# Kernel tuning notes

Measured on AMD Instinct MI355X. Metric: run time of the kernel, lower is better.

Reference implementation:

```python
import jax, jax.numpy as jnp
import numpy as np

NHEAD = 8

def setup_inputs() -> dict:
    key = jax.random.key(0)
    ks = jax.random.split(key, 6)
    b, n, d = 4, 1024, 512
    emb = jax.random.normal(ks[0], (b, n, d), dtype=jnp.float32)
    dirs = jax.random.normal(ks[1], (b, n, n, 3), dtype=jnp.float32)
    d_mask = jax.random.normal(ks[2], (b * NHEAD, n, n), dtype=jnp.float32) * 0.1
    W_proj = jax.random.normal(ks[3], (d, 3 * d), dtype=jnp.float32) / np.sqrt(d)
    b_proj = jnp.zeros((3 * d,), dtype=jnp.float32)
    w_force = jax.random.normal(ks[4], (d,), dtype=jnp.float32) / np.sqrt(d)
    b_force = jnp.zeros((1,), dtype=jnp.float32)
    return {"emb": emb, "dirs": dirs, "d_mask": d_mask, "W_proj": W_proj,
            "b_proj": b_proj, "w_force": w_force, "b_force": b_force}

def reference(emb, dirs, d_mask, W_proj, b_proj, w_force, b_force):
    b, n, d = emb.shape
    h = NHEAD
    dh = d // h
    scale = jnp.asarray(np.sqrt(d), emb.dtype)
    qkv = emb @ W_proj + b_proj                      # (b,n,3d)
    q, k, v = jnp.split(qkv, 3, axis=-1)
    q = q.reshape(b, n, h, dh).transpose(0, 2, 1, 3) / scale   # (b,h,n,dh)
    k = k.reshape(b, n, h, dh).transpose(0, 2, 1, 3)           # (b,h,n,dh)
    v = v.reshape(b, n, h, dh).transpose(0, 2, 1, 3)           # (b,h,n,dh)
    scores = jnp.einsum('bhid,bhjd->bhij', q, k) + d_mask.reshape(b, h, n, n)
    attn = jax.nn.softmax(scores, axis=-1)                     # (b,h,n,n); dropout in eval mode = identity
    # torch: (attn[...,None] * dirs[:,None]) @ v  materializes (b,h,n,n,3);
    # fused einsum computes the same per-axis weighted sum without it.
    xyz = jnp.einsum('bhij,bija,bhjd->biahd', attn, dirs, v)   # (b,n,3,h,dh)
    xyz = xyz.reshape(b, n, 3, d)
    out = jnp.einsum('bnad,d->bna', xyz, w_force) + b_force[0]  # (b,n,3)
    return out
```

## Files before the change

kernel.cpp:

```cpp
#include <hip/hip_runtime.h>
#include <hip/hip_bf16.h>

#define NH 8
#define BB 4
#define NN 1024
#define DD 512
#define DH 64
#define JSPLIT 8

typedef __bf16 bf16x8 __attribute__((ext_vector_type(8)));
typedef float f32x4 __attribute__((ext_vector_type(4)));

__device__ __forceinline__ unsigned short f2bf(float f) {
    union { float f; unsigned u; } v; v.f = f;
    unsigned u = v.u;
    unsigned r = u + 0x7FFFu + ((u >> 16) & 1u);
    return (unsigned short)(r >> 16);
}

__global__ __launch_bounds__(256) void k_prep(const float* __restrict__ W,
                                              const float* __restrict__ b_proj,
                                              const float* __restrict__ w_force,
                                              unsigned short* __restrict__ Wt,
                                              float* __restrict__ bias_eff,
                                              float* __restrict__ wv_eff,
                                              float* __restrict__ s_bias) {
    __shared__ float tile[32][33];
    int bx = blockIdx.x;
    int t = threadIdx.x;
    const float rscale = 0.044194173824159216f;
    if (bx < 512) {
        int c0 = (bx & 15) * 32;
        int n0 = (bx >> 4) * 32;
        for (int i = 0; i < 4; ++i) {
            int idx = t + i * 256;
            int r = idx >> 5, cn = idx & 31;
            tile[r][cn] = W[(c0 + r) * (3 * DD) + n0 + cn];
        }
        __syncthreads();
        for (int i = 0; i < 4; ++i) {
            int idx = t + i * 256;
            int nn = idx >> 5, cc = idx & 31;
            float v = tile[cc][nn];
            int n = n0 + nn;
            if (n < DD) v *= rscale;
            Wt[n * DD + c0 + cc] = f2bf(v);
        }
        if ((bx & 15) == 0 && t < 32) {
            int n = n0 + t;
            bias_eff[n] = b_proj[n] * (n < DD ? rscale : 1.0f);
        }
        return;
    }
    int wave = t >> 6, lane = t & 63;
    if (bx == 640) {
        if (wave == 0) {
            for (int hh = 0; hh < NH; ++hh) {
                float p = b_proj[2 * DD + hh * DH + lane] * w_force[hh * DH + lane];
                for (int off = 32; off; off >>= 1) p += __shfl_xor(p, off);
                if (lane == 0) s_bias[hh] = p;
            }
        }
        return;
    }
    int c = (bx - 512) * 4 + wave;
    const float* wr = W + (size_t)c * (3 * DD) + 2 * DD;
    #pragma unroll
    for (int hh = 0; hh < NH; ++hh) {
        float p = wr[hh * DH + lane] * w_force[hh * DH + lane];
        for (int off = 32; off; off >>= 1) p += __shfl_xor(p, off);
        if (lane == 0) wv_eff[c * 8 + hh] = p;
    }
}

__global__ __launch_bounds__(128) void k_s(const float* __restrict__ emb,
                                           const float* __restrict__ wv_eff,
                                           const float* __restrict__ s_bias,
                                           float* __restrict__ s_ws) {
    int t = blockIdx.x * 128 + threadIdx.x;
    int row = t >> 3;
    int h = t & 7;
    const float* er = emb + (size_t)row * DD;
    const float* wp = wv_eff + h;
    float acc = 0.f;
    #pragma unroll 8
    for (int c4 = 0; c4 < DD / 4; ++c4) {
        float4 e = *(const float4*)(er + c4 * 4);
        acc += e.x * wp[(c4 * 4 + 0) * 8];
        acc += e.y * wp[(c4 * 4 + 1) * 8];
        acc += e.z * wp[(c4 * 4 + 2) * 8];
        acc += e.w * wp[(c4 * 4 + 3) * 8];
    }
    int b = row >> 10, j = row & 1023;
    s_ws[(b * 8 + h) * NN + j] = acc + s_bias[h];
}

__global__ __launch_bounds__(256) void k_gemm(const float* __restrict__ emb,
                                              const unsigned short* __restrict__ Wt,
                                              const float* __restrict__ bias_eff,
                                              unsigned short* __restrict__ qb,
                                              unsigned short* __restrict__ kb) {
    __shared__ __align__(16) unsigned short a_s[128 * 32];
    __shared__ __align__(16) unsigned short b_s[128 * 32];
    int m0 = blockIdx.x * 128, n0 = blockIdx.y * 128;
    int t = threadIdx.x;
    int wave = t >> 6, lane = t & 63;
    int wr = (wave >> 1) * 64, wc = (wave & 1) * 64;
    int qd = lane >> 4, c = lane & 15;
    int sr = t >> 2, sg = (t & 3) * 8;
    f32x4 acc[4][4] = {};
    for (int k0 = 0; k0 < DD; k0 += 32) {
        float4 x0 = *(const float4*)(emb + (size_t)(m0 + sr) * DD + k0 + sg);
        float4 x1 = *(const float4*)(emb + (size_t)(m0 + sr) * DD + k0 + sg + 4);
        float4 y0 = *(const float4*)(emb + (size_t)(m0 + 64 + sr) * DD + k0 + sg);
        float4 y1 = *(const float4*)(emb + (size_t)(m0 + 64 + sr) * DD + k0 + sg + 4);
        uint4 bv0 = *(const uint4*)(Wt + (size_t)(n0 + sr) * DD + k0 + sg);
        uint4 bv1 = *(const uint4*)(Wt + (size_t)(n0 + 64 + sr) * DD + k0 + sg);
        union { unsigned short u[8]; uint4 v; } px, py;
        px.u[0] = f2bf(x0.x); px.u[1] = f2bf(x0.y); px.u[2] = f2bf(x0.z); px.u[3] = f2bf(x0.w);
        px.u[4] = f2bf(x1.x); px.u[5] = f2bf(x1.y); px.u[6] = f2bf(x1.z); px.u[7] = f2bf(x1.w);
        py.u[0] = f2bf(y0.x); py.u[1] = f2bf(y0.y); py.u[2] = f2bf(y0.z); py.u[3] = f2bf(y0.w);
        py.u[4] = f2bf(y1.x); py.u[5] = f2bf(y1.y); py.u[6] = f2bf(y1.z); py.u[7] = f2bf(y1.w);
        __syncthreads();
        *(uint4*)(&a_s[sr * 32 + sg]) = px.v;
        *(uint4*)(&a_s[(64 + sr) * 32 + sg]) = py.v;
        *(uint4*)(&b_s[sr * 32 + sg]) = bv0;
        *(uint4*)(&b_s[(64 + sr) * 32 + sg]) = bv1;
        __syncthreads();
        bf16x8 af[4], bfr[4];
        #pragma unroll
        for (int mi = 0; mi < 4; ++mi)
            af[mi] = *(const bf16x8*)(&a_s[(wr + mi * 16 + c) * 32 + qd * 8]);
        #pragma unroll
        for (int ni = 0; ni < 4; ++ni)
            bfr[ni] = *(const bf16x8*)(&b_s[(wc + ni * 16 + c) * 32 + qd * 8]);
        #pragma unroll
        for (int mi = 0; mi < 4; ++mi)
            #pragma unroll
            for (int ni = 0; ni < 4; ++ni)
                acc[mi][ni] = __builtin_amdgcn_mfma_f32_16x16x32_bf16(af[mi], bfr[ni], acc[mi][ni], 0, 0, 0);
    }
    bool isQ = (n0 < DD);
    unsigned short* dst = isQ ? qb : kb;
    int nb = isQ ? n0 : n0 - DD;
    #pragma unroll
    for (int mi = 0; mi < 4; ++mi)
        #pragma unroll
        for (int ni = 0; ni < 4; ++ni) {
            int col = nb + wc + ni * 16 + c;
            float be = bias_eff[isQ ? col : col + DD];
            #pragma unroll
            for (int r = 0; r < 4; ++r) {
                int row = m0 + wr + mi * 16 + qd * 4 + r;
                dst[(size_t)row * DD + col] = f2bf(acc[mi][ni][r] + be);
            }
        }
}

__global__ __launch_bounds__(512, 4) void k_attn(const unsigned short* __restrict__ qb,
                                                 const unsigned short* __restrict__ kb,
                                                 const float* __restrict__ s_ws,
                                                 const float* __restrict__ d_mask,
                                                 const float* __restrict__ dirs,
                                                 float* __restrict__ part) {
    int blk = blockIdx.x;
    int itile = blk & 63;
    int rest = blk >> 6;
    int b = rest & 3;
    int chunk = rest >> 2;
    int i0 = itile * 16;
    int j_base = chunk * (NN / JSPLIT);
    int t = threadIdx.x;
    int h = t >> 6;
    int lane = t & 63, qd = lane >> 4, c = lane & 15;
    int i = i0 + c;

    const unsigned short* qbase = qb + ((size_t)(b * NN + i) * DD + h * DH + qd * 8);
    bf16x8 aq0 = *(const bf16x8*)(qbase);
    bf16x8 aq1 = *(const bf16x8*)(qbase + 32);

    const unsigned short* kp = kb + ((size_t)(b * NN + j_base + c) * DD + h * DH + qd * 8);
    const float* mp = d_mask + (size_t)(b * NH + h) * NN * NN + (size_t)i * NN + j_base + qd * 4;
    const float* sp = s_ws + (b * NH + h) * NN + j_base + qd * 4;
    const float* dp = dirs + (((size_t)b * NN + i) * NN + j_base + qd * 4) * 3;

    float acc0 = 0.f, acc1 = 0.f, acc2 = 0.f, l = 0.f;

    bf16x8 ck0 = *(const bf16x8*)(kp);
    bf16x8 ck1 = *(const bf16x8*)(kp + 32);
    f32x4 cmk = __builtin_nontemporal_load((const f32x4*)mp);
    f32x4 csj = *(const f32x4*)sp;
    f32x4 cd0 = *(const f32x4*)(dp);
    f32x4 cd1 = *(const f32x4*)(dp + 4);
    f32x4 cd2 = *(const f32x4*)(dp + 8);

    auto step = [&](bf16x8 k0, bf16x8 k1, f32x4 mk, f32x4 sj, f32x4 d0, f32x4 d1, f32x4 d2) {
        f32x4 sc = {0.f, 0.f, 0.f, 0.f};
        sc = __builtin_amdgcn_mfma_f32_16x16x32_bf16(k0, aq0, sc, 0, 0, 0);
        sc = __builtin_amdgcn_mfma_f32_16x16x32_bf16(k1, aq1, sc, 0, 0, 0);
        float p0 = __expf(sc[0] + mk.x);
        float p1 = __expf(sc[1] + mk.y);
        float p2 = __expf(sc[2] + mk.z);
        float p3 = __expf(sc[3] + mk.w);
        l += p0 + p1 + p2 + p3;
        float t0 = p0 * sj.x, t1 = p1 * sj.y, t2 = p2 * sj.z, t3 = p3 * sj.w;
        acc0 += t0 * d0.x + t1 * d0.w + t2 * d1.z + t3 * d2.y;
        acc1 += t0 * d0.y + t1 * d1.x + t2 * d1.w + t3 * d2.z;
        acc2 += t0 * d0.z + t1 * d1.y + t2 * d2.x + t3 * d2.w;
    };

    #pragma unroll
    for (int it = 0; it < NN / JSPLIT / 16 - 1; ++it) {
        kp += 16 * DD; mp += 16; sp += 16; dp += 48;
        bf16x8 nk0 = *(const bf16x8*)(kp);
        bf16x8 nk1 = *(const bf16x8*)(kp + 32);
        f32x4 nmk = __builtin_nontemporal_load((const f32x4*)mp);
        f32x4 nsj = *(const f32x4*)sp;
        f32x4 nd0 = *(const f32x4*)(dp);
        f32x4 nd1 = *(const f32x4*)(dp + 4);
        f32x4 nd2 = *(const f32x4*)(dp + 8);
        step(ck0, ck1, cmk, csj, cd0, cd1, cd2);
        ck0 = nk0; ck1 = nk1; cmk = nmk; csj = nsj; cd0 = nd0; cd1 = nd1; cd2 = nd2;
    }
    step(ck0, ck1, cmk, csj, cd0, cd1, cd2);

    l    += __shfl_xor(l, 16);    l    += __shfl_xor(l, 32);
    acc0 += __shfl_xor(acc0, 16); acc0 += __shfl_xor(acc0, 32);
    acc1 += __shfl_xor(acc1, 16); acc1 += __shfl_xor(acc1, 32);
    acc2 += __shfl_xor(acc2, 16); acc2 += __shfl_xor(acc2, 32);
    if (qd == 0) {
        f32x4 o; o[0] = l; o[1] = acc0; o[2] = acc1; o[3] = acc2;
        *(f32x4*)(part + ((((size_t)(chunk * BB + b)) * NH + h) * NN + i) * 4) = o;
    }
}

__global__ __launch_bounds__(256) void k_fin(const float4* __restrict__ part,
                                             const float* __restrict__ b_force,
                                             float* __restrict__ out) {
    int t = blockIdx.x * 256 + threadIdx.x;
    int b = t >> 10, i = t & 1023;
    float o0, o1, o2;
    o0 = o1 = o2 = b_force[0];
    #pragma unroll
    for (int h = 0; h < NH; ++h) {
        float lx = 0.f, a0 = 0.f, a1 = 0.f, a2 = 0.f;
        #pragma unroll
        for (int ch = 0; ch < JSPLIT; ++ch) {
            float4 p = part[(((size_t)(ch * BB + b) * NH + h) * NN) + i];
            lx += p.x; a0 += p.y; a1 += p.z; a2 += p.w;
        }
        float inv = 1.0f / lx;
        o0 += a0 * inv; o1 += a1 * inv; o2 += a2 * inv;
    }
    out[t * 3 + 0] = o0;
    out[t * 3 + 1] = o1;
    out[t * 3 + 2] = o2;
}

extern "C" void kernel_launch(void* const* d_in, const int* in_sizes, int n_in,
                              void* d_out, int out_size, void* d_ws, size_t ws_size,
                              hipStream_t stream) {
    (void)in_sizes; (void)n_in; (void)out_size; (void)ws_size;
    const float* emb     = (const float*)d_in[0];
    const float* dirs    = (const float*)d_in[1];
    const float* d_mask  = (const float*)d_in[2];
    const float* W       = (const float*)d_in[3];
    const float* b_proj  = (const float*)d_in[4];
    const float* w_force = (const float*)d_in[5];
    const float* b_force = (const float*)d_in[6];
    float* out = (float*)d_out;

    char* ws = (char*)d_ws;
    float* wv_eff   = (float*)ws;
    float* s_bias   = wv_eff + 4096;
    float* bias_eff = s_bias + 8;
    float* s_ws     = bias_eff + 1024;
    unsigned short* Wt = (unsigned short*)(s_ws + 32768);
    unsigned short* qb = Wt + 1024 * 512;
    unsigned short* kb = qb + 4096 * 512;
    float* part = (float*)(kb + 4096 * 512);

    hipLaunchKernelGGL(k_prep, dim3(641),     dim3(256), 0, stream,
                       W, b_proj, w_force, Wt, bias_eff, wv_eff, s_bias);
    hipLaunchKernelGGL(k_s,    dim3(256),     dim3(128), 0, stream, emb, wv_eff, s_bias, s_ws);
    hipLaunchKernelGGL(k_gemm, dim3(32, 8),   dim3(256), 0, stream, emb, Wt, bias_eff, qb, kb);
    hipLaunchKernelGGL(k_attn, dim3(BB * 64 * JSPLIT), dim3(512), 0, stream,
                       qb, kb, s_ws, d_mask, dirs, part);
    hipLaunchKernelGGL(k_fin,  dim3(16),      dim3(256), 0, stream, (const float4*)part, b_force, out);
}
```

Baseline: 345.7 us.

## Restructure attention: per-head blocks, stage scores in LDS, row-coalesced mask/dirs reads

The attention kernel now gives each block one (batch, head, 16-row tile) instead of splitting j into 8 chunks across heads. It first computes QK^T scores with MFMA into shared memory as bf16. In a second phase each wave reads full rows of d_mask and dirs with contiguous lane-wise float4 loads, so the loads coalesce better, and it reduces across the wave. This removes the JSPLIT partial sums and simplifies the final kernel. The cost is an extra rounding of scores to bf16, a block barrier, and reading dirs once per head instead of once for all heads together, which is 8x more dirs traffic.

```diff
diff --git a/kernel.cpp b/kernel.cpp
--- a/kernel.cpp
+++ b/kernel.cpp
@@ -6,7 +6,7 @@
 #define NN 1024
 #define DD 512
 #define DH 64
-#define JSPLIT 8
+#define SCS 1032
 
 typedef __bf16 bf16x8 __attribute__((ext_vector_type(8)));
 typedef float f32x4 __attribute__((ext_vector_type(4)));
@@ -16,6 +16,9 @@
     unsigned u = v.u;
     unsigned r = u + 0x7FFFu + ((u >> 16) & 1u);
     return (unsigned short)(r >> 16);
+}
+__device__ __forceinline__ float b2f(unsigned short u) {
+    union { unsigned u; float f; } cv; cv.u = ((unsigned)u) << 16; return cv.f;
 }
 
 __global__ __launch_bounds__(256) void k_prep(const float* __restrict__ W,
@@ -157,80 +160,86 @@
         }
 }
 
-__global__ __launch_bounds__(512, 4) void k_attn(const unsigned short* __restrict__ qb,
-                                                 const unsigned short* __restrict__ kb,
-                                                 const float* __restrict__ s_ws,
-                                                 const float* __restrict__ d_mask,
-                                                 const float* __restrict__ dirs,
-                                                 float* __restrict__ part) {
+__global__ __launch_bounds__(256) void k_attn(const unsigned short* __restrict__ qb,
+                                              const unsigned short* __restrict__ kb,
+                                              const float* __restrict__ s_ws,
+                                              const float* __restrict__ d_mask,
+                                              const float* __restrict__ dirs,
+                                              float* __restrict__ part) {
+    __shared__ unsigned short sc_s[16 * SCS];
     int blk = blockIdx.x;
     int itile = blk & 63;
-    int rest = blk >> 6;
-    int b = rest & 3;
-    int chunk = rest >> 2;
+    int bh = blk >> 6;
+    int h = bh & 7;
+    int b = bh >> 3;
     int i0 = itile * 16;
-    int j_base = chunk * (NN / JSPLIT);
     int t = threadIdx.x;
-    int h = t >> 6;
-    int lane = t & 63, qd = lane >> 4, c = lane & 15;
-    int i = i0 + c;
-
-    const unsigned short* qbase = qb + ((size_t)(b * NN + i) * DD + h * DH + qd * 8);
+    int w = t >> 6, lane = t & 63, qd = lane >> 4, c = lane & 15;
+
+    const unsigned short* qbase = qb + ((size_t)(b * NN + i0 + c) * DD + h * DH + qd * 8);
     bf16x8 aq0 = *(const bf16x8*)(qbase);
     bf16x8 aq1 = *(const bf16x8*)(qbase + 32);
-
-    const unsigned short* kp = kb + ((size_t)(b * NN + j_base + c) * DD + h * DH + qd * 8);
-    const float* mp = d_mask + (size_t)(b * NH + h) * NN * NN + (size_t)i * NN + j_base + qd * 4;
-    const float* sp = s_ws + (b * NH + h) * NN + j_base + qd * 4;
-    const float* dp = dirs + (((size_t)b * NN + i) * NN + j_base + qd * 4) * 3;
-
-    float acc0 = 0.f, acc1 = 0.f, acc2 = 0.f, l = 0.f;
-
-    bf16x8 ck0 = *(const bf16x8*)(kp);
-    bf16x8 ck1 = *(const bf16x8*)(kp + 32);
-    f32x4 cmk = __builtin_nontemporal_load((const f32x4*)mp);
-    f32x4 csj = *(const f32x4*)sp;
-    f32x4 cd0 = *(const f32x4*)(dp);
-    f32x4 cd1 = *(const f32x4*)(dp + 4);
-    f32x4 cd2 = *(const f32x4*)(dp + 8);
-
-    auto step = [&](bf16x8 k0, bf16x8 k1, f32x4 mk, f32x4 sj, f32x4 d0, f32x4 d1, f32x4 d2) {
+    int j0w = w * 256;
+    #pragma unroll
+    for (int jt = 0; jt < 16; ++jt) {
+        int j0 = j0w + jt * 16;
+        const unsigned short* kba = kb + ((size_t)(b * NN + j0 + c) * DD + h * DH + qd * 8);
+        bf16x8 kf0 = *(const bf16x8*)(kba);
+        bf16x8 kf1 = *(const bf16x8*)(kba + 32);
         f32x4 sc = {0.f, 0.f, 0.f, 0.f};
-        sc = __builtin_amdgcn_mfma_f32_16x16x32_bf16(k0, aq0, sc, 0, 0, 0);
-        sc = __builtin_amdgcn_mfma_f32_16x16x32_bf16(k1, aq1, sc, 0, 0, 0);
-        float p0 = __expf(sc[0] + mk.x);
-        float p1 = __expf(sc[1] + mk.y);
-        float p2 = __expf(sc[2] + mk.z);
-        float p3 = __expf(sc[3] + mk.w);
-        l += p0 + p1 + p2 + p3;
-        float t0 = p0 * sj.x, t1 = p1 * sj.y, t2 = p2 * sj.z, t3 = p3 * sj.w;
-        acc0 += t0 * d0.x + t1 * d0.w + t2 * d1.z + t3 * d2.y;
-        acc1 += t0 * d0.y + t1 * d1.x + t2 * d1.w + t3 * d2.z;
-        acc2 += t0 * d0.z + t1 * d1.y + t2 * d2.x + t3 * d2.w;
-    };
-
-    #pragma unroll
-    for (int it = 0; it < NN / JSPLIT / 16 - 1; ++it) {
-        kp += 16 * DD; mp += 16; sp += 16; dp += 48;
-        bf16x8 nk0 = *(const bf16x8*)(kp);
-        bf16x8 nk1 = *(const bf16x8*)(kp + 32);
-        f32x4 nmk = __builtin_nontemporal_load((const f32x4*)mp);
-        f32x4 nsj = *(const f32x4*)sp;
-        f32x4 nd0 = *(const f32x4*)(dp);
-        f32x4 nd1 = *(const f32x4*)(dp + 4);
-        f32x4 nd2 = *(const f32x4*)(dp + 8);
-        step(ck0, ck1, cmk, csj, cd0, cd1, cd2);
-        ck0 = nk0; ck1 = nk1; cmk = nmk; csj = nsj; cd0 = nd0; cd1 = nd1; cd2 = nd2;
-    }
-    step(ck0, ck1, cmk, csj, cd0, cd1, cd2);
-
-    l    += __shfl_xor(l, 16);    l    += __shfl_xor(l, 32);
-    acc0 += __shfl_xor(acc0, 16); acc0 += __shfl_xor(acc0, 32);
-    acc1 += __shfl_xor(acc1, 16); acc1 += __shfl_xor(acc1, 32);
-    acc2 += __shfl_xor(acc2, 16); acc2 += __shfl_xor(acc2, 32);
-    if (qd == 0) {
-        f32x4 o; o[0] = l; o[1] = acc0; o[2] = acc1; o[3] = acc2;
-        *(f32x4*)(part + ((((size_t)(chunk * BB + b)) * NH + h) * NN + i) * 4) = o;
+        sc = __builtin_amdgcn_mfma_f32_16x16x32_bf16(kf0, aq0, sc, 0, 0, 0);
+        sc = __builtin_amdgcn_mfma_f32_16x16x32_bf16(kf1, aq1, sc, 0, 0, 0);
+        ushort4 pk;
+        pk.x = f2bf(sc[0]); pk.y = f2bf(sc[1]); pk.z = f2bf(sc[2]); pk.w = f2bf(sc[3]);
+        *(ushort4*)(&sc_s[c * SCS + j0 + qd * 4]) = pk;
+    }
+    __syncthreads();
+
+    const float* sm = s_ws + bh * NN;
+    float4 sv[4];
+    #pragma unroll
+    for (int seg = 0; seg < 4; ++seg)
+        sv[seg] = *(const float4*)(sm + seg * 256 + lane * 4);
+
+    const float* mbase = d_mask + (size_t)bh * NN * NN;
+    const float* dbase = dirs + (size_t)b * NN * NN * 3;
+
+    #pragma unroll
+    for (int r4 = 0; r4 < 4; ++r4) {
+        int il = w * 4 + r4;
+        int i = i0 + il;
+        const float* mrow = mbase + (size_t)i * NN + lane * 4;
+        const float* drow = dbase + ((size_t)i * NN + lane * 4) * 3;
+        float l = 0.f, a0 = 0.f, a1 = 0.f, a2 = 0.f;
+        #pragma unroll
+        for (int seg = 0; seg < 4; ++seg) {
+            float4 mk = *(const float4*)(mrow + seg * 256);
+            float4 d0 = *(const float4*)(drow + seg * 768);
+            float4 d1 = *(const float4*)(drow + seg * 768 + 4);
+            float4 d2 = *(const float4*)(drow + seg * 768 + 8);
+            ushort4 scv = *(const ushort4*)(&sc_s[il * SCS + seg * 256 + lane * 4]);
+            float p0 = __expf(b2f(scv.x) + mk.x);
+            float p1 = __expf(b2f(scv.y) + mk.y);
+            float p2 = __expf(b2f(scv.z) + mk.z);
+            float p3 = __expf(b2f(scv.w) + mk.w);
+            l += p0 + p1 + p2 + p3;
+            float t0 = p0 * sv[seg].x, t1 = p1 * sv[seg].y;
+            float t2 = p2 * sv[seg].z, t3 = p3 * sv[seg].w;
+            a0 += t0 * d0.x + t1 * d0.w + t2 * d1.z + t3 * d2.y;
+            a1 += t0 * d0.y + t1 * d1.x + t2 * d1.w + t3 * d2.z;
+            a2 += t0 * d0.z + t1 * d1.y + t2 * d2.x + t3 * d2.w;
+        }
+        #pragma unroll
+        for (int off = 1; off < 64; off <<= 1) {
+            l  += __shfl_xor(l, off);
+            a0 += __shfl_xor(a0, off);
+            a1 += __shfl_xor(a1, off);
+            a2 += __shfl_xor(a2, off);
+        }
+        if (lane == 0) {
+            f32x4 o; o[0] = l; o[1] = a0; o[2] = a1; o[3] = a2;
+            *(f32x4*)(part + ((size_t)bh * NN + i) * 4) = o;
+        }
     }
 }
 
@@ -243,14 +252,9 @@
     o0 = o1 = o2 = b_force[0];
     #pragma unroll
     for (int h = 0; h < NH; ++h) {
-        float lx = 0.f, a0 = 0.f, a1 = 0.f, a2 = 0.f;
-        #pragma unroll
-        for (int ch = 0; ch < JSPLIT; ++ch) {
-            float4 p = part[(((size_t)(ch * BB + b) * NH + h) * NN) + i];
-            lx += p.x; a0 += p.y; a1 += p.z; a2 += p.w;
-        }
-        float inv = 1.0f / lx;
-        o0 += a0 * inv; o1 += a1 * inv; o2 += a2 * inv;
+        float4 p = part[(((size_t)(b * NH + h)) << 10) + i];
+        float inv = 1.0f / p.x;
+        o0 += p.y * inv; o1 += p.z * inv; o2 += p.w * inv;
     }
     out[t * 3 + 0] = o0;
     out[t * 3 + 1] = o1;
@@ -280,11 +284,11 @@
     unsigned short* kb = qb + 4096 * 512;
     float* part = (float*)(kb + 4096 * 512);
 
-    hipLaunchKernelGGL(k_prep, dim3(641),     dim3(256), 0, stream,
+    hipLaunchKernelGGL(k_prep, dim3(641),      dim3(256), 0, stream,
                        W, b_proj, w_force, Wt, bias_eff, wv_eff, s_bias);
-    hipLaunchKernelGGL(k_s,    dim3(256),     dim3(128), 0, stream, emb, wv_eff, s_bias, s_ws);
-    hipLaunchKernelGGL(k_gemm, dim3(32, 8),   dim3(256), 0, stream, emb, Wt, bias_eff, qb, kb);
-    hipLaunchKernelGGL(k_attn, dim3(BB * 64 * JSPLIT), dim3(512), 0, stream,
+    hipLaunchKernelGGL(k_s,    dim3(256),      dim3(128), 0, stream, emb, wv_eff, s_bias, s_ws);
+    hipLaunchKernelGGL(k_gemm, dim3(32, 8),    dim3(256), 0, stream, emb, Wt, bias_eff, qb, kb);
+    hipLaunchKernelGGL(k_attn, dim3(BB * NH * 64), dim3(256), 0, stream,
                        qb, kb, s_ws, d_mask, dirs, part);
-    hipLaunchKernelGGL(k_fin,  dim3(16),      dim3(256), 0, stream, (const float4*)part, b_force, out);
-}
+    hipLaunchKernelGGL(k_fin,  dim3(16),       dim3(256), 0, stream, (const float4*)part, b_force, out);
+}
```

Measured after the change: 314.0 us. 1.1x faster.
